# Performance work log

Hardware: AMD Instinct MI355X
Metric: run time of the kernel (lower is better)

Reference implementation:

```python
import jax, jax.numpy as jnp
import numpy as np

NHEADS = 8
HEAD_DIM = 64  # odim // nheads = 512 // 8


def setup_inputs() -> dict:
    key = jax.random.key(0)
    ks = jax.random.split(key, 5)
    B, S, D = 2, 4096, 512
    scale = 1.0 / np.sqrt(D)
    return {
        "m_feats": jax.random.normal(ks[0], (B, S, D), dtype=jnp.float32),
        "Wc": jax.random.normal(ks[1], (2 * D, D), dtype=jnp.float32) * scale,
        "bc": jax.random.normal(ks[2], (2 * D,), dtype=jnp.float32) * 0.01,
        "Wv": jax.random.normal(ks[3], (D, D), dtype=jnp.float32) * scale,
        "bv": jax.random.normal(ks[4], (D,), dtype=jnp.float32) * 0.01,
    }


def reference(m_feats, Wc, bc, Wv, bv):
    # eval mode: dropout(p=0.5) is identity
    B, S, D = m_feats.shape
    H, Dh = NHEADS, HEAD_DIM
    m_k = m_feats @ Wv.T + bv                    # [B,S,D]
    m_trans = m_feats @ Wc.T + bc                # [B,S,2D]
    m_q, m_v = m_trans[..., :D], m_trans[..., D:]
    # torch.split into contiguous per-head chunks == reshape to [B,S,H,Dh]
    k = m_k.reshape(B, S, H, Dh)
    q = m_q.reshape(B, S, H, Dh)
    v = m_v.reshape(B, S, H, Dh)
    # scores[b,h,i,j] = k_i . q_j / sqrt(Dh); softmax over j (the q axis)
    scores = jnp.einsum("bihd,bjhd->bhij", k, q) / np.sqrt(Dh).astype(np.float32)
    w = jax.nn.softmax(scores, axis=-1)          # [B,H,S,S]
    r = jnp.einsum("bhij,bjhd->bihd", w, v).reshape(B, S, D)
    return m_feats + r
```

## Files before the change

kernel.cpp:

```cpp
#include <hip/hip_runtime.h>

#define MTOT 8192

typedef __attribute__((ext_vector_type(8))) short bf16x8;
typedef __attribute__((ext_vector_type(4))) float f32x4;

#if __has_builtin(__builtin_amdgcn_exp2f)
#define EXP2F __builtin_amdgcn_exp2f
#else
#define EXP2F exp2f
#endif

#define SC 0.18033688011112042f
#define LDP 72
#define CTS 136

static __device__ __forceinline__ unsigned short tb(float f) {
  union { float f; unsigned int i; } x;
  x.f = f;
  return (unsigned short)(x.i >> 16);
}
static __device__ __forceinline__ unsigned int pkt(float a, float b) {
  union { float f; unsigned int i; } xa, xb;
  xa.f = a; xb.f = b;
  return (xa.i >> 16) | (xb.i & 0xFFFF0000u);
}
static __device__ __forceinline__ bf16x8 ld8f32_bf16(const float* __restrict__ p) {
  f32x4 lo = *(const f32x4*)p;
  f32x4 hi = *(const f32x4*)(p + 4);
  union { unsigned int u[4]; bf16x8 v; } r;
  r.u[0] = pkt(lo[0], lo[1]);
  r.u[1] = pkt(lo[2], lo[3]);
  r.u[2] = pkt(hi[0], hi[1]);
  r.u[3] = pkt(hi[2], hi[3]);
  return r.v;
}

__global__ __launch_bounds__(256) void gemm_qvk(
    const float* __restrict__ mf,
    const float* __restrict__ Wc,
    const float* __restrict__ bc,
    const float* __restrict__ Wv,
    const float* __restrict__ bv,
    unsigned short* __restrict__ ws,
    int nct)
{
  const int cpx = (int)gridDim.x >> 3;
  const int bid = ((int)blockIdx.x & 7) * cpx + ((int)blockIdx.x >> 3);
  const int tn = bid % nct, tm = bid / nct;
  const int w = threadIdx.x >> 6, lane = threadIdx.x & 63;
  const int n = lane & 15, q = lane >> 4;

  __shared__ alignas(16) unsigned short smem[2 * 128 * LDP];
  unsigned short* As = smem;
  unsigned short* Bs = smem + 128 * LDP;

  f32x4 acc[4][4] = {};
  const int rowA0 = tm * 128, colB0 = tn * 128;
  const int sr = threadIdx.x >> 4;
  const int sc = (threadIdx.x & 15) * 4;

  for (int kc = 0; kc < 512; kc += 64) {
    __syncthreads();
#pragma unroll
    for (int rr = 0; rr < 8; ++rr) {
      const int row = rr * 16 + sr;
      f32x4 av = *(const f32x4*)(mf + (size_t)(rowA0 + row) * 512 + kc + sc);
      uint2 ap; ap.x = pkt(av[0], av[1]); ap.y = pkt(av[2], av[3]);
      *(uint2*)(&As[row * LDP + sc]) = ap;
      const int c = colB0 + row;
      const float* bsrc = (c < 1024) ? (Wc + (size_t)c * 512)
                                     : (Wv + (size_t)(c - 1024) * 512);
      f32x4 bvx = *(const f32x4*)(bsrc + kc + sc);
      uint2 bp; bp.x = pkt(bvx[0], bvx[1]); bp.y = pkt(bvx[2], bvx[3]);
      *(uint2*)(&Bs[row * LDP + sc]) = bp;
    }
    __syncthreads();
#pragma unroll
    for (int ks = 0; ks < 2; ++ks) {
      bf16x8 a[4], b[4];
#pragma unroll
      for (int si = 0; si < 4; ++si)
        a[si] = *(const bf16x8*)(&As[((w >> 1) * 64 + si * 16 + n) * LDP + ks * 32 + q * 8]);
#pragma unroll
      for (int sj = 0; sj < 4; ++sj)
        b[sj] = *(const bf16x8*)(&Bs[((w & 1) * 64 + sj * 16 + n) * LDP + ks * 32 + q * 8]);
#pragma unroll
      for (int si = 0; si < 4; ++si)
#pragma unroll
        for (int sj = 0; sj < 4; ++sj)
          acc[si][sj] = __builtin_amdgcn_mfma_f32_16x16x32_bf16(a[si], b[sj], acc[si][sj], 0, 0, 0);
    }
  }

  __syncthreads();
  unsigned short* Ct = smem;
  const bool isV = (tn >= 4 && tn < 8);
  const int rl0 = (w >> 1) * 64, cl0 = (w & 1) * 64;

  if (!isV) {
    const bool isK = (tn >= 8);
#pragma unroll
    for (int sj = 0; sj < 4; ++sj) {
      const int c = colB0 + sj * 16 + n;
      const float bias = isK ? bv[c - 1024] : bc[c];
#pragma unroll
      for (int si = 0; si < 4; ++si)
#pragma unroll
        for (int r = 0; r < 4; ++r) {
          float v = acc[si][sj][r] + bias;
          if (isK) v *= SC;
          Ct[(rl0 + si * 16 + q * 4 + r) * CTS + cl0 + sj * 16 + n] = tb(v);
        }
    }
  } else {
#pragma unroll
    for (int sj = 0; sj < 4; ++sj) {
      const float bias = bc[colB0 + sj * 16 + n];
#pragma unroll
      for (int si = 0; si < 4; ++si) {
        uint2 pk;
        pk.x = pkt(acc[si][sj][0] + bias, acc[si][sj][1] + bias);
        pk.y = pkt(acc[si][sj][2] + bias, acc[si][sj][3] + bias);
        *(uint2*)(&Ct[(cl0 + sj * 16 + n) * CTS + rl0 + si * 16 + q * 4]) = pk;
      }
    }
  }
  __syncthreads();

  const int rk = threadIdx.x & 7, rr2 = threadIdx.x >> 3;
#pragma unroll
  for (int rp = 0; rp < 4; ++rp) {
    const int row = rp * 32 + rr2;
#pragma unroll
    for (int ch = 0; ch < 2; ++ch) {
      const int col = ch * 64 + rk * 8;
      bf16x8 v = *(const bf16x8*)(&Ct[row * CTS + col]);
      if (!isV) {
        const int srow = rowA0 + row;
        const int bb = srow >> 12, ss = srow & 4095;
        const int cg = colB0 + col;
        const int cl = (cg >= 1024) ? (cg - 1024) : cg;
        const int hh = cl >> 6, dh0 = cl & 63;
        unsigned short* base = (cg >= 1024) ? (ws + (size_t)2 * MTOT * 512) : ws;
        *(bf16x8*)(base + ((size_t)((bb * 8 + hh) * 4096 + ss)) * 64 + dh0) = v;
      } else {
        const int cv = (tn - 4) * 128 + row;
        const int hh = cv >> 6, dh0 = cv & 63;
        const int sg = rowA0 + col;
        const int bb = sg >> 12, ss = sg & 4095;
        *(bf16x8*)(ws + (size_t)MTOT * 512 +
                   ((size_t)((bb * 8 + hh) * 64 + dh0)) * 4096 + ss) = v;
      }
    }
  }
}

template <bool KWS>
__global__ __launch_bounds__(128, 2) void attn_kernel(
    const unsigned short* __restrict__ qvws,
    const float* __restrict__ mf,
    const float* __restrict__ Wv,
    const float* __restrict__ bv,
    float* __restrict__ out)
{
  const int bid = blockIdx.x;
  const int bh = ((bid & 7) << 1) | ((bid >> 3) & 1);
  const int ib = bid >> 4;
  const int b_ = bh >> 3, h = bh & 7;
  const int w = threadIdx.x >> 6, lane = threadIdx.x & 63;
  const int n = lane & 15, q = lane >> 4;
  const int i0 = ib * 64;

  __shared__ alignas(16) unsigned short PK[2][64 * LDP];
  __shared__ float lbuf[2][64];

  const unsigned short* Qb = qvws + (size_t)(bh * 4096) * 64;
  const unsigned short* Vb = qvws + (size_t)MTOT * 512 + (size_t)(bh * 64) * 4096;

  bf16x8 aK[4][2];
  if (KWS) {
    const unsigned short* Kb = qvws + (size_t)2 * MTOT * 512 + (size_t)(bh * 4096) * 64;
#pragma unroll
    for (int sub = 0; sub < 4; ++sub)
#pragma unroll
      for (int s = 0; s < 2; ++s)
        aK[sub][s] = *(const bf16x8*)(Kb + (size_t)(i0 + sub * 16 + n) * 64 + s * 32 + q * 8);
  } else {
    f32x4 ka[2][4] = {};
    for (int kk = 0; kk < 512; kk += 32) {
      bf16x8 a0 = ld8f32_bf16(mf + (size_t)(b_ * 4096 + i0 + (2 * w + 0) * 16 + n) * 512 + kk + q * 8);
      bf16x8 a1 = ld8f32_bf16(mf + (size_t)(b_ * 4096 + i0 + (2 * w + 1) * 16 + n) * 512 + kk + q * 8);
#pragma unroll
      for (int t = 0; t < 4; ++t) {
        bf16x8 bw = ld8f32_bf16(Wv + (size_t)(h * 64 + t * 16 + n) * 512 + kk + q * 8);
        ka[0][t] = __builtin_amdgcn_mfma_f32_16x16x32_bf16(a0, bw, ka[0][t], 0, 0, 0);
        ka[1][t] = __builtin_amdgcn_mfma_f32_16x16x32_bf16(a1, bw, ka[1][t], 0, 0, 0);
      }
    }
#pragma unroll
    for (int sl = 0; sl < 2; ++sl)
#pragma unroll
      for (int t = 0; t < 4; ++t) {
        const float bias = bv[h * 64 + t * 16 + n];
#pragma unroll
        for (int r = 0; r < 4; ++r)
          PK[0][((2 * w + sl) * 16 + q * 4 + r) * LDP + t * 16 + n] =
              tb((ka[sl][t][r] + bias) * SC);
      }
    __syncthreads();
#pragma unroll
    for (int sub = 0; sub < 4; ++sub)
#pragma unroll
      for (int s = 0; s < 2; ++s)
        aK[sub][s] = *(const bf16x8*)(&PK[0][(sub * 16 + n) * LDP + s * 32 + q * 8]);
    __syncthreads();
  }

  f32x4 o[4][4] = {};
  float lsc[4] = {0.0f, 0.0f, 0.0f, 0.0f};
  unsigned short* Pw = &PK[w][0];
  const int jbase = w * 2048;

  bf16x8 bq[4][2], bvv[4][2];
#pragma unroll
  for (int jt = 0; jt < 4; ++jt)
#pragma unroll
    for (int s = 0; s < 2; ++s)
      bq[jt][s] = *(const bf16x8*)(Qb + (size_t)(jbase + jt * 16 + n) * 64 + s * 32 + q * 8);
#pragma unroll
  for (int t = 0; t < 4; ++t)
#pragma unroll
    for (int s = 0; s < 2; ++s)
      bvv[t][s] = *(const bf16x8*)(Vb + (size_t)(t * 16 + n) * 4096 + jbase + s * 32 + q * 8);

  for (int it = 0; it < 32; ++it) {
    const int j1 = jbase + ((it + 1) & 31) * 64;

    f32x4 c[2][4];
#pragma unroll
    for (int jt = 0; jt < 4; ++jt) {
      f32x4 z = {};
      z = __builtin_amdgcn_mfma_f32_16x16x32_bf16(bq[jt][0], aK[0][0], z, 0, 0, 0);
      z = __builtin_amdgcn_mfma_f32_16x16x32_bf16(bq[jt][1], aK[0][1], z, 0, 0, 0);
      c[0][jt] = z;
    }

#pragma unroll
    for (int sub = 0; sub < 4; ++sub) {
      const int cur = sub & 1, nxt = cur ^ 1;
      if (sub < 3) {
#pragma unroll
        for (int jt = 0; jt < 4; ++jt) {
          f32x4 z = {};
          z = __builtin_amdgcn_mfma_f32_16x16x32_bf16(bq[jt][0], aK[sub + 1][0], z, 0, 0, 0);
          z = __builtin_amdgcn_mfma_f32_16x16x32_bf16(bq[jt][1], aK[sub + 1][1], z, 0, 0, 0);
          c[nxt][jt] = z;
        }
      }
      if (sub == 2) {
#pragma unroll
        for (int jt = 0; jt < 4; ++jt)
#pragma unroll
          for (int s = 0; s < 2; ++s)
            bq[jt][s] = *(const bf16x8*)(Qb + (size_t)(j1 + jt * 16 + n) * 64 + s * 32 + q * 8);
      }

#pragma unroll
      for (int jt = 0; jt < 4; ++jt) {
        float e0 = EXP2F(c[cur][jt][0]), e1 = EXP2F(c[cur][jt][1]);
        float e2 = EXP2F(c[cur][jt][2]), e3 = EXP2F(c[cur][jt][3]);
        lsc[sub] += (e0 + e1) + (e2 + e3);
        uint2 pk;
        pk.x = pkt(e0, e1);
        pk.y = pkt(e2, e3);
        *(uint2*)(Pw + (sub * 16 + n) * LDP + jt * 16 + q * 4) = pk;
      }

      asm volatile("s_waitcnt lgkmcnt(0)" ::: "memory");

#pragma unroll
      for (int s = 0; s < 2; ++s) {
        bf16x8 pa = *(const bf16x8*)(Pw + (sub * 16 + n) * LDP + s * 32 + q * 8);
#pragma unroll
        for (int t = 0; t < 4; ++t)
          o[sub][t] = __builtin_amdgcn_mfma_f32_16x16x32_bf16(pa, bvv[t][s], o[sub][t], 0, 0, 0);
      }
    }

#pragma unroll
    for (int t = 0; t < 4; ++t)
#pragma unroll
      for (int s = 0; s < 2; ++s)
        bvv[t][s] = *(const bf16x8*)(Vb + (size_t)(t * 16 + n) * 4096 + j1 + s * 32 + q * 8);
  }

  float lw[4];
#pragma unroll
  for (int sub = 0; sub < 4; ++sub) {
    float v = lsc[sub];
    v += __shfl_xor(v, 16, 64);
    v += __shfl_xor(v, 32, 64);
    lw[sub] = v;
  }

  __syncthreads();
  float* mO = (float*)&PK[0][0];
  const int ebase = (w == 0) ? 0 : 32;
  const int rbase = (w == 0) ? 32 : 0;
  const int esub0 = (w == 0) ? 2 : 0;
  const int ksub0 = (w == 0) ? 0 : 2;
#pragma unroll
  for (int sl = 0; sl < 2; ++sl) {
    const int sub = esub0 + sl;
#pragma unroll
    for (int t = 0; t < 4; ++t)
#pragma unroll
      for (int r = 0; r < 4; ++r)
        mO[(ebase + sl * 16 + q * 4 + r) * 68 + t * 16 + n] = o[sub][t][r];
  }
  if (lane < 16) {
#pragma unroll
    for (int sub = 0; sub < 4; ++sub)
      lbuf[w][sub * 16 + lane] = lw[sub];
  }
  __syncthreads();
#pragma unroll
  for (int sl = 0; sl < 2; ++sl) {
    const int sub = ksub0 + sl;
    float li[4];
#pragma unroll
    for (int r = 0; r < 4; ++r) {
      const int il = sub * 16 + q * 4 + r;
      li[r] = 1.0f / (lbuf[0][il] + lbuf[1][il]);
    }
#pragma unroll
    for (int t = 0; t < 4; ++t) {
#pragma unroll
      for (int r = 0; r < 4; ++r) {
        const int i = i0 + sub * 16 + q * 4 + r;
        const int dh = t * 16 + n;
        const size_t idx = (size_t)(b_ * 4096 + i) * 512 + h * 64 + dh;
        out[idx] = (o[sub][t][r] + mO[(rbase + sl * 16 + q * 4 + r) * 68 + t * 16 + n]) * li[r]
                   + mf[idx];
      }
    }
  }
}

extern "C" void kernel_launch(void* const* d_in, const int* in_sizes, int n_in,
                              void* d_out, int out_size, void* d_ws, size_t ws_size,
                              hipStream_t stream) {
  const float* mf = (const float*)d_in[0];
  const float* Wc = (const float*)d_in[1];
  const float* bc = (const float*)d_in[2];
  const float* Wv = (const float*)d_in[3];
  const float* bv = (const float*)d_in[4];
  float* out = (float*)d_out;
  unsigned short* ws = (unsigned short*)d_ws;

  const bool kws = ws_size >= (size_t)3 * MTOT * 512 * 2;
  const int nct = kws ? 12 : 8;

  gemm_qvk<<<64 * nct, 256, 0, stream>>>(mf, Wc, bc, Wv, bv, ws, nct);
  if (kws)
    attn_kernel<true><<<1024, 128, 0, stream>>>(ws, mf, Wv, bv, out);
  else
    attn_kernel<false><<<1024, 128, 0, stream>>>(ws, mf, Wv, bv, out);
}
```

Before: 240.8 us.

## Pre-convert inputs to bf16 and stage GEMM tiles via direct global-to-LDS loads

Adds a separate kernel that converts m_feats, Wc and Wv to bf16 in workspace. A new GEMM then loads the bf16 tiles straight into LDS with global_load_lds, so the fp32 loads and per-tile packing leave the GEMM inner loop. This costs an extra launch plus an extra write and read of the converted operands. The LDS tiles lose their padding (stride 64 instead of 72), which can cause bank conflicts on the MFMA operand reads. It only runs when the workspace is large enough.

After: 237.2 us. Within noise of the previous version (-1.5%).

```diff
diff --git a/kernel.cpp b/kernel.cpp
--- a/kernel.cpp
+++ b/kernel.cpp
@@ -36,44 +36,74 @@
   return r.v;
 }
 
-__global__ __launch_bounds__(256) void gemm_qvk(
+static __device__ __forceinline__ void stage16(const unsigned short* g,
+                                               unsigned short* l, int lane) {
+#if __has_builtin(__builtin_amdgcn_global_load_lds)
+  __builtin_amdgcn_global_load_lds(
+      (const __attribute__((address_space(1))) void*)g,
+      (__attribute__((address_space(3))) void*)l, 16, 0, 0);
+#else
+  *(uint4*)(l + lane * 8) = *(const uint4*)g;
+#endif
+}
+
+__global__ __launch_bounds__(256) void convert_bf16(
     const float* __restrict__ mf,
     const float* __restrict__ Wc,
+    const float* __restrict__ Wv,
+    unsigned short* __restrict__ dst)
+{
+  const size_t NA = (size_t)MTOT * 512;
+  const size_t NW = (size_t)1536 * 512;
+  const size_t total = (NA + NW) / 8;
+  for (size_t u = (size_t)blockIdx.x * blockDim.x + threadIdx.x; u < total;
+       u += (size_t)gridDim.x * blockDim.x) {
+    const size_t el = u * 8;
+    const float* src;
+    if (el < NA) {
+      src = mf + el;
+    } else {
+      const size_t e2 = el - NA;
+      src = (e2 < (size_t)1024 * 512) ? (Wc + e2) : (Wv + (e2 - (size_t)1024 * 512));
+    }
+    f32x4 lo = *(const f32x4*)src;
+    f32x4 hi = *(const f32x4*)(src + 4);
+    uint4 pk;
+    pk.x = pkt(lo[0], lo[1]); pk.y = pkt(lo[2], lo[3]);
+    pk.z = pkt(hi[0], hi[1]); pk.w = pkt(hi[2], hi[3]);
+    *(uint4*)(dst + el) = pk;
+  }
+}
+
+__global__ __launch_bounds__(256) void gemm_fast(
+    const unsigned short* __restrict__ Abf,
+    const unsigned short* __restrict__ Wbf,
     const float* __restrict__ bc,
-    const float* __restrict__ Wv,
     const float* __restrict__ bv,
-    unsigned short* __restrict__ ws,
-    int nct)
+    unsigned short* __restrict__ ws)
 {
   const int cpx = (int)gridDim.x >> 3;
   const int bid = ((int)blockIdx.x & 7) * cpx + ((int)blockIdx.x >> 3);
-  const int tn = bid % nct, tm = bid / nct;
+  const int tn = bid % 12, tm = bid / 12;
   const int w = threadIdx.x >> 6, lane = threadIdx.x & 63;
   const int n = lane & 15, q = lane >> 4;
 
   __shared__ alignas(16) unsigned short smem[2 * 128 * LDP];
   unsigned short* As = smem;
-  unsigned short* Bs = smem + 128 * LDP;
+  unsigned short* Bs = smem + 128 * 64;
 
   f32x4 acc[4][4] = {};
   const int rowA0 = tm * 128, colB0 = tn * 128;
-  const int sr = threadIdx.x >> 4;
-  const int sc = (threadIdx.x & 15) * 4;
+  const int lr = lane >> 3;
+  const int lc = (lane & 7) * 8;
+  const unsigned short* gA = Abf + (size_t)(rowA0 + w * 32 + lr) * 512 + lc;
+  const unsigned short* gB = Wbf + (size_t)(colB0 + w * 32 + lr) * 512 + lc;
 
   for (int kc = 0; kc < 512; kc += 64) {
-    __syncthreads();
-#pragma unroll
-    for (int rr = 0; rr < 8; ++rr) {
-      const int row = rr * 16 + sr;
-      f32x4 av = *(const f32x4*)(mf + (size_t)(rowA0 + row) * 512 + kc + sc);
-      uint2 ap; ap.x = pkt(av[0], av[1]); ap.y = pkt(av[2], av[3]);
-      *(uint2*)(&As[row * LDP + sc]) = ap;
-      const int c = colB0 + row;
-      const float* bsrc = (c < 1024) ? (Wc + (size_t)c * 512)
-                                     : (Wv + (size_t)(c - 1024) * 512);
-      f32x4 bvx = *(const f32x4*)(bsrc + kc + sc);
-      uint2 bp; bp.x = pkt(bvx[0], bvx[1]); bp.y = pkt(bvx[2], bvx[3]);
-      *(uint2*)(&Bs[row * LDP + sc]) = bp;
+#pragma unroll
+    for (int rr = 0; rr < 4; ++rr) {
+      stage16(gA + (size_t)rr * 8 * 512 + kc, As + (w * 32 + rr * 8) * 64, lane);
+      stage16(gB + (size_t)rr * 8 * 512 + kc, Bs + (w * 32 + rr * 8) * 64, lane);
     }
     __syncthreads();
 #pragma unroll
@@ -81,19 +111,19 @@
       bf16x8 a[4], b[4];
 #pragma unroll
       for (int si = 0; si < 4; ++si)
-        a[si] = *(const bf16x8*)(&As[((w >> 1) * 64 + si * 16 + n) * LDP + ks * 32 + q * 8]);
+        a[si] = *(const bf16x8*)(&As[((w >> 1) * 64 + si * 16 + n) * 64 + ks * 32 + q * 8]);
 #pragma unroll
       for (int sj = 0; sj < 4; ++sj)
-        b[sj] = *(const bf16x8*)(&Bs[((w & 1) * 64 + sj * 16 + n) * LDP + ks * 32 + q * 8]);
+        b[sj] = *(const bf16x8*)(&Bs[((w & 1) * 64 + sj * 16 + n) * 64 + ks * 32 + q * 8]);
 #pragma unroll
       for (int si = 0; si < 4; ++si)
 #pragma unroll
         for (int sj = 0; sj < 4; ++sj)
           acc[si][sj] = __builtin_amdgcn_mfma_f32_16x16x32_bf16(a[si], b[sj], acc[si][sj], 0, 0, 0);
     }
-  }
-
-  __syncthreads();
+    __syncthreads();
+  }
+
   unsigned short* Ct = smem;
   const bool isV = (tn >= 4 && tn < 8);
   const int rl0 = (w >> 1) * 64, cl0 = (w & 1) * 64;
@@ -156,6 +186,126 @@
   }
 }
 
+__global__ __launch_bounds__(256) void gemm_qvk(
+    const float* __restrict__ mf,
+    const float* __restrict__ Wc,
+    const float* __restrict__ bc,
+    const float* __restrict__ Wv,
+    const float* __restrict__ bv,
+    unsigned short* __restrict__ ws,
+    int nct)
+{
+  const int cpx = (int)gridDim.x >> 3;
+  const int bid = ((int)blockIdx.x & 7) * cpx + ((int)blockIdx.x >> 3);
+  const int tn = bid % nct, tm = bid / nct;
+  const int w = threadIdx.x >> 6, lane = threadIdx.x & 63;
+  const int n = lane & 15, q = lane >> 4;
+
+  __shared__ alignas(16) unsigned short smem[2 * 128 * LDP];
+  unsigned short* As = smem;
+  unsigned short* Bs = smem + 128 * LDP;
+
+  f32x4 acc[4][4] = {};
+  const int rowA0 = tm * 128, colB0 = tn * 128;
+  const int sr = threadIdx.x >> 4;
+  const int sc = (threadIdx.x & 15) * 4;
+
+  for (int kc = 0; kc < 512; kc += 64) {
+    __syncthreads();
+#pragma unroll
+    for (int rr = 0; rr < 8; ++rr) {
+      const int row = rr * 16 + sr;
+      f32x4 av = *(const f32x4*)(mf + (size_t)(rowA0 + row) * 512 + kc + sc);
+      uint2 ap; ap.x = pkt(av[0], av[1]); ap.y = pkt(av[2], av[3]);
+      *(uint2*)(&As[row * LDP + sc]) = ap;
+      const int c = colB0 + row;
+      const float* bsrc = (c < 1024) ? (Wc + (size_t)c * 512)
+                                     : (Wv + (size_t)(c - 1024) * 512);
+      f32x4 bvx = *(const f32x4*)(bsrc + kc + sc);
+      uint2 bp; bp.x = pkt(bvx[0], bvx[1]); bp.y = pkt(bvx[2], bvx[3]);
+      *(uint2*)(&Bs[row * LDP + sc]) = bp;
+    }
+    __syncthreads();
+#pragma unroll
+    for (int ks = 0; ks < 2; ++ks) {
+      bf16x8 a[4], b[4];
+#pragma unroll
+      for (int si = 0; si < 4; ++si)
+        a[si] = *(const bf16x8*)(&As[((w >> 1) * 64 + si * 16 + n) * LDP + ks * 32 + q * 8]);
+#pragma unroll
+      for (int sj = 0; sj < 4; ++sj)
+        b[sj] = *(const bf16x8*)(&Bs[((w & 1) * 64 + sj * 16 + n) * LDP + ks * 32 + q * 8]);
+#pragma unroll
+      for (int si = 0; si < 4; ++si)
+#pragma unroll
+        for (int sj = 0; sj < 4; ++sj)
+          acc[si][sj] = __builtin_amdgcn_mfma_f32_16x16x32_bf16(a[si], b[sj], acc[si][sj], 0, 0, 0);
+    }
+  }
+
+  __syncthreads();
+  unsigned short* Ct = smem;
+  const bool isV = (tn >= 4 && tn < 8);
+  const int rl0 = (w >> 1) * 64, cl0 = (w & 1) * 64;
+
+  if (!isV) {
+    const bool isK = (tn >= 8);
+#pragma unroll
+    for (int sj = 0; sj < 4; ++sj) {
+      const int c = colB0 + sj * 16 + n;
+      const float bias = isK ? bv[c - 1024] : bc[c];
+#pragma unroll
+      for (int si = 0; si < 4; ++si)
+#pragma unroll
+        for (int r = 0; r < 4; ++r) {
+          float v = acc[si][sj][r] + bias;
+          if (isK) v *= SC;
+          Ct[(rl0 + si * 16 + q * 4 + r) * CTS + cl0 + sj * 16 + n] = tb(v);
+        }
+    }
+  } else {
+#pragma unroll
+    for (int sj = 0; sj < 4; ++sj) {
+      const float bias = bc[colB0 + sj * 16 + n];
+#pragma unroll
+      for (int si = 0; si < 4; ++si) {
+        uint2 pk;
+        pk.x = pkt(acc[si][sj][0] + bias, acc[si][sj][1] + bias);
+        pk.y = pkt(acc[si][sj][2] + bias, acc[si][sj][3] + bias);
+        *(uint2*)(&Ct[(cl0 + sj * 16 + n) * CTS + rl0 + si * 16 + q * 4]) = pk;
+      }
+    }
+  }
+  __syncthreads();
+
+  const int rk = threadIdx.x & 7, rr2 = threadIdx.x >> 3;
+#pragma unroll
+  for (int rp = 0; rp < 4; ++rp) {
+    const int row = rp * 32 + rr2;
+#pragma unroll
+    for (int ch = 0; ch < 2; ++ch) {
+      const int col = ch * 64 + rk * 8;
+      bf16x8 v = *(const bf16x8*)(&Ct[row * CTS + col]);
+      if (!isV) {
+        const int srow = rowA0 + row;
+        const int bb = srow >> 12, ss = srow & 4095;
+        const int cg = colB0 + col;
+        const int cl = (cg >= 1024) ? (cg - 1024) : cg;
+        const int hh = cl >> 6, dh0 = cl & 63;
+        unsigned short* base = (cg >= 1024) ? (ws + (size_t)2 * MTOT * 512) : ws;
+        *(bf16x8*)(base + ((size_t)((bb * 8 + hh) * 4096 + ss)) * 64 + dh0) = v;
+      } else {
+        const int cv = (tn - 4) * 128 + row;
+        const int hh = cv >> 6, dh0 = cv & 63;
+        const int sg = rowA0 + col;
+        const int bb = sg >> 12, ss = sg & 4095;
+        *(bf16x8*)(ws + (size_t)MTOT * 512 +
+                   ((size_t)((bb * 8 + hh) * 64 + dh0)) * 4096 + ss) = v;
+      }
+    }
+  }
+}
+
 template <bool KWS>
 __global__ __launch_bounds__(128, 2) void attn_kernel(
     const unsigned short* __restrict__ qvws,
@@ -359,12 +509,22 @@
   float* out = (float*)d_out;
   unsigned short* ws = (unsigned short*)d_ws;
 
-  const bool kws = ws_size >= (size_t)3 * MTOT * 512 * 2;
-  const int nct = kws ? 12 : 8;
-
-  gemm_qvk<<<64 * nct, 256, 0, stream>>>(mf, Wc, bc, Wv, bv, ws, nct);
-  if (kws)
+  const size_t elQ = (size_t)MTOT * 512;
+  const size_t needFast = ((size_t)4 * MTOT * 512 + (size_t)1536 * 512) * 2;
+  const bool fast = ws_size >= needFast;
+  const bool kws = ws_size >= (size_t)3 * elQ * 2;
+
+  if (fast) {
+    unsigned short* Abf = ws + 3 * elQ;
+    unsigned short* Wbf = ws + 4 * elQ;
+    convert_bf16<<<2048, 256, 0, stream>>>(mf, Wc, Wv, Abf);
+    gemm_fast<<<768, 256, 0, stream>>>(Abf, Wbf, bc, bv, ws);
     attn_kernel<true><<<1024, 128, 0, stream>>>(ws, mf, Wv, bv, out);
-  else
+  } else if (kws) {
+    gemm_qvk<<<64 * 12, 256, 0, stream>>>(mf, Wc, bc, Wv, bv, ws, 12);
+    attn_kernel<true><<<1024, 128, 0, stream>>>(ws, mf, Wv, bv, out);
+  } else {
+    gemm_qvk<<<64 * 8, 256, 0, stream>>>(mf, Wc, bc, Wv, bv, ws, 8);
     attn_kernel<false><<<1024, 128, 0, stream>>>(ws, mf, Wv, bv, out);
-}
+  }
+}
```
